# Kernel tuning notes

Hardware: AMD Instinct MI355X
Metric: run time of the kernel (lower is better)

Reference implementation:

```python
import jax, jax.numpy as jnp
import numpy as np

H = 128

def setup_inputs() -> dict:
    key = jax.random.key(0)
    kx, ke, ku, kub, kv, kvb = jax.random.split(key, 6)
    B, N = 8, 256
    s = 1.0 / np.sqrt(H)
    return {
        "x": jax.random.normal(kx, (B, N, H), dtype=jnp.float32),
        "e": jax.random.normal(ke, (B, N, N, H), dtype=jnp.float32),
        "U_w": jax.random.uniform(ku, (H, H), jnp.float32, -s, s),
        "U_b": jax.random.uniform(kub, (H,), jnp.float32, -s, s),
        "V_w": jax.random.uniform(kv, (H, H), jnp.float32, -s, s),
        "V_b": jax.random.uniform(kvb, (H,), jnp.float32, -s, s),
    }

def reference(x, e, U_w, U_b, V_w, V_b):
    # Ue: [B,N,N,H] = Linear(e); Vx: [B,N,H] = Linear(x)
    Ue = jnp.einsum('bijh,oh->bijo', e, U_w) + U_b
    Vx = jnp.einsum('bnh,oh->bno', x, V_w) + V_b
    # e_new[b,i,j] = Ue[b,i,j] + Vx[b,i] (rows) + Vx[b,j] (cols)
    e_new = Ue + Vx[:, :, None, :] + Vx[:, None, :, :]
    return e_new
```

## Files before the change

### kernel.cpp

```cpp
#include <hip/hip_runtime.h>
#include <hip/hip_bf16.h>


#define LDB 136

using bf16x8 = __attribute__((ext_vector_type(8))) short;
using f32x4  = __attribute__((ext_vector_type(4))) float;

__device__ inline bf16x8 pack8(const float4 a, const float4 b) {
  union { __hip_bfloat162 h2[4]; bf16x8 v; } u;
  u.h2[0] = __float22bfloat162_rn(make_float2(a.x, a.y));
  u.h2[1] = __float22bfloat162_rn(make_float2(a.z, a.w));
  u.h2[2] = __float22bfloat162_rn(make_float2(b.x, b.y));
  u.h2[3] = __float22bfloat162_rn(make_float2(b.z, b.w));
  return u.v;
}

__global__ __launch_bounds__(256) void vx_kernel(
    const float* __restrict__ x, const float* __restrict__ Vw,
    const float* __restrict__ Vb, const float* __restrict__ Ub,
    float* __restrict__ vx2) {
  __shared__ float xs[8][128];
  const int r0 = blockIdx.x * 8;
  for (int i = threadIdx.x; i < 8 * 32; i += 256)
    ((float4*)&xs[0][0])[i] = ((const float4*)(x + (size_t)r0 * 128))[i];
  __syncthreads();

  const int o    = threadIdx.x & 127;
  const int half = threadIdx.x >> 7;
  float acc[4] = {0.f, 0.f, 0.f, 0.f};
  const float4* vwrow = (const float4*)(Vw + (size_t)o * 128);
#pragma unroll 4
  for (int kc = 0; kc < 32; ++kc) {
    const float4 w4 = vwrow[kc];
#pragma unroll
    for (int r = 0; r < 4; ++r) {
      const float4 xv = ((const float4*)&xs[half * 4 + r][0])[kc];
      acc[r] += xv.x * w4.x + xv.y * w4.y + xv.z * w4.z + xv.w * w4.w;
    }
  }
  const float bias = Vb[o] + 0.5f * Ub[o];
#pragma unroll
  for (int r = 0; r < 4; ++r)
    vx2[(size_t)(r0 + half * 4 + r) * 128 + o] = acc[r] + bias;
}

__global__ __launch_bounds__(256) void edge_kernel(
    const float* __restrict__ e, const float* __restrict__ Uw,
    const float* __restrict__ vx2, float* __restrict__ out) {
  __shared__ alignas(16) __hip_bfloat16 As[64 * LDB];

  const int tid  = threadIdx.x;
  const int wave = tid >> 6;
  const int lane = tid & 63;
  const int ln   = lane & 15;
  const int kg   = lane >> 4;

  bf16x8 bfrag[2][4];
#pragma unroll
  for (int c = 0; c < 2; ++c) {
    const int o = 32 * wave + 16 * c + ln;
#pragma unroll
    for (int ks = 0; ks < 4; ++ks) {
      const float4* p = (const float4*)(Uw + (size_t)o * 128 + kg * 8 + ks * 32);
      bfrag[c][ks] = pack8(p[0], p[1]);
    }
  }

  const int nTiles = (8 * 256 * 256) / 64;
  for (int t = blockIdx.x; t < nTiles; t += gridDim.x) {
    const size_t rowBase = (size_t)t * 64;

    {
      const float4* src = (const float4*)(e + rowBase * 128);
      float4 f[8];
#pragma unroll
      for (int i = 0; i < 8; ++i) f[i] = src[i * 256 + tid];
#pragma unroll
      for (int i = 0; i < 8; ++i) {
        const int fi  = i * 256 + tid;
        const int row = fi >> 5;
        const int col = (fi & 31) * 4;
        union { __hip_bfloat162 h2[2]; unsigned long long u; } p;
        p.h2[0] = __float22bfloat162_rn(make_float2(f[i].x, f[i].y));
        p.h2[1] = __float22bfloat162_rn(make_float2(f[i].z, f[i].w));
        *(unsigned long long*)&As[row * LDB + col] = p.u;
      }
    }
    __syncthreads();

    f32x4 acc[4][2];
#pragma unroll
    for (int sub = 0; sub < 4; ++sub) {
      bf16x8 afrag[4];
#pragma unroll
      for (int ks = 0; ks < 4; ++ks)
        afrag[ks] = *(const bf16x8*)&As[(sub * 16 + ln) * LDB + kg * 8 + ks * 32];
#pragma unroll
      for (int c = 0; c < 2; ++c) {
        f32x4 a = {0.f, 0.f, 0.f, 0.f};
#pragma unroll
        for (int ks = 0; ks < 4; ++ks)
          a = __builtin_amdgcn_mfma_f32_16x16x32_bf16(afrag[ks], bfrag[c][ks], a, 0, 0, 0);
        acc[sub][c] = a;
      }
    }

#pragma unroll
    for (int sub = 0; sub < 4; ++sub) {
      const size_t rsub = rowBase + sub * 16;
      const int bi = (int)(rsub >> 8);
      const int b_ = (int)(rsub >> 16);
      const int j0 = (int)(rsub & 255);
      const int jr = b_ * 256 + j0;
#pragma unroll
      for (int c = 0; c < 2; ++c) {
        const int o = 32 * wave + 16 * c + ln;
        const float vxi = vx2[(size_t)bi * 128 + o];
#pragma unroll
        for (int reg = 0; reg < 4; ++reg) {
          const int rr = kg * 4 + reg;
          const float vxj = vx2[(size_t)(jr + rr) * 128 + o];
          out[(rsub + rr) * 128 + o] = acc[sub][c][reg] + vxi + vxj;
        }
      }
    }
    __syncthreads();
  }
}

extern "C" void kernel_launch(void* const* d_in, const int* in_sizes, int n_in,
                              void* d_out, int out_size, void* d_ws, size_t ws_size,
                              hipStream_t stream) {
  const float* x  = (const float*)d_in[0];
  const float* e  = (const float*)d_in[1];
  const float* Uw = (const float*)d_in[2];
  const float* Ub = (const float*)d_in[3];
  const float* Vw = (const float*)d_in[4];
  const float* Vb = (const float*)d_in[5];
  float* out = (float*)d_out;
  float* vx2 = (float*)d_ws;

  vx_kernel<<<256, 256, 0, stream>>>(x, Vw, Vb, Ub, vx2);
  edge_kernel<<<2048, 256, 0, stream>>>(e, Uw, vx2, out);
}
```

Before: 457.4 us.

## Give each wave an independent 16-row strip, loading A fragments straight into registers

The edge kernel no longer stages e tiles through LDS behind block-wide barriers. Each wave now owns 16-row strips, loads its A fragments directly from global memory into registers, and computes all 128 output columns. The U weights are held in LDS as pre-swizzled fragments, and the accumulators are seeded with the Vx row and column terms so no epilogue add is needed. This removes the per-tile __syncthreads and the LDS round-trip for the activations. The cost is more uncoalesced 32-byte global reads per lane and fewer rows in flight per block.

```diff
diff --git a/kernel.cpp b/kernel.cpp
--- a/kernel.cpp
+++ b/kernel.cpp
@@ -1,8 +1,6 @@
 #include <hip/hip_runtime.h>
 #include <hip/hip_bf16.h>
 
-
-#define LDB 136
 
 using bf16x8 = __attribute__((ext_vector_type(8))) short;
 using f32x4  = __attribute__((ext_vector_type(4))) float;
@@ -48,84 +46,79 @@
 __global__ __launch_bounds__(256) void edge_kernel(
     const float* __restrict__ e, const float* __restrict__ Uw,
     const float* __restrict__ vx2, float* __restrict__ out) {
-  __shared__ alignas(16) __hip_bfloat16 As[64 * LDB];
+  __shared__ alignas(16) bf16x8 Bs[8 * 4 * 64];
 
-  const int tid  = threadIdx.x;
+  const int tid = threadIdx.x;
+
+#pragma unroll
+  for (int k = 0; k < 8; ++k) {
+    const int idx  = tid + k * 256;
+    const int ll   = idx & 63;
+    const int ksi  = (idx >> 6) & 3;
+    const int cgi  = idx >> 8;
+    const int o    = cgi * 16 + (ll & 15);
+    const int kq   = ll >> 4;
+    const float4* p = (const float4*)(Uw + (size_t)o * 128 + ksi * 32 + kq * 8);
+    Bs[idx] = pack8(p[0], p[1]);
+  }
+  __syncthreads();
+
   const int wave = tid >> 6;
   const int lane = tid & 63;
   const int ln   = lane & 15;
   const int kg   = lane >> 4;
 
-  bf16x8 bfrag[2][4];
-#pragma unroll
-  for (int c = 0; c < 2; ++c) {
-    const int o = 32 * wave + 16 * c + ln;
+  const int gw = blockIdx.x * 4 + wave;
+  const int nw = gridDim.x * 4;
+  const int nStrips = (8 * 256 * 256) / 16;
+
+  for (int s = gw; s < nStrips; s += nw) {
+    const size_t rowBase = (size_t)s * 16;
+    const int bi = (int)(rowBase >> 8);
+    const int b_ = (int)(rowBase >> 16);
+    const int j0 = (int)(rowBase & 255);
+    const int jr = b_ * 256 + j0;
+
+    const float* arow = e + (rowBase + ln) * 128 + kg * 8;
+    float4 a0[4], a1[4];
 #pragma unroll
     for (int ks = 0; ks < 4; ++ks) {
-      const float4* p = (const float4*)(Uw + (size_t)o * 128 + kg * 8 + ks * 32);
-      bfrag[c][ks] = pack8(p[0], p[1]);
+      a0[ks] = *(const float4*)(arow + ks * 32);
+      a1[ks] = *(const float4*)(arow + ks * 32 + 4);
     }
-  }
 
-  const int nTiles = (8 * 256 * 256) / 64;
-  for (int t = blockIdx.x; t < nTiles; t += gridDim.x) {
-    const size_t rowBase = (size_t)t * 64;
+    f32x4 acc[8];
+#pragma unroll
+    for (int cg = 0; cg < 8; ++cg) {
+      const int o = cg * 16 + ln;
+      const float vxi = vx2[(size_t)bi * 128 + o];
+      const float* vj = vx2 + (size_t)(jr + kg * 4) * 128 + o;
+#pragma unroll
+      for (int reg = 0; reg < 4; ++reg)
+        acc[cg][reg] = vxi + vj[reg * 128];
+    }
 
-    {
-      const float4* src = (const float4*)(e + rowBase * 128);
-      float4 f[8];
+    bf16x8 af[4];
 #pragma unroll
-      for (int i = 0; i < 8; ++i) f[i] = src[i * 256 + tid];
+    for (int ks = 0; ks < 4; ++ks) af[ks] = pack8(a0[ks], a1[ks]);
+
 #pragma unroll
-      for (int i = 0; i < 8; ++i) {
-        const int fi  = i * 256 + tid;
-        const int row = fi >> 5;
-        const int col = (fi & 31) * 4;
-        union { __hip_bfloat162 h2[2]; unsigned long long u; } p;
-        p.h2[0] = __float22bfloat162_rn(make_float2(f[i].x, f[i].y));
-        p.h2[1] = __float22bfloat162_rn(make_float2(f[i].z, f[i].w));
-        *(unsigned long long*)&As[row * LDB + col] = p.u;
-      }
-    }
-    __syncthreads();
-
-    f32x4 acc[4][2];
-#pragma unroll
-    for (int sub = 0; sub < 4; ++sub) {
-      bf16x8 afrag[4];
+    for (int cg = 0; cg < 8; ++cg) {
+      const bf16x8* bp = &Bs[cg * 4 * 64 + lane];
+      f32x4 a = acc[cg];
 #pragma unroll
       for (int ks = 0; ks < 4; ++ks)
-        afrag[ks] = *(const bf16x8*)&As[(sub * 16 + ln) * LDB + kg * 8 + ks * 32];
-#pragma unroll
-      for (int c = 0; c < 2; ++c) {
-        f32x4 a = {0.f, 0.f, 0.f, 0.f};
-#pragma unroll
-        for (int ks = 0; ks < 4; ++ks)
-          a = __builtin_amdgcn_mfma_f32_16x16x32_bf16(afrag[ks], bfrag[c][ks], a, 0, 0, 0);
-        acc[sub][c] = a;
-      }
+        a = __builtin_amdgcn_mfma_f32_16x16x32_bf16(af[ks], bp[ks * 64], a, 0, 0, 0);
+      acc[cg] = a;
     }
 
+    float* orow = out + (rowBase + kg * 4) * 128 + ln;
 #pragma unroll
-    for (int sub = 0; sub < 4; ++sub) {
-      const size_t rsub = rowBase + sub * 16;
-      const int bi = (int)(rsub >> 8);
-      const int b_ = (int)(rsub >> 16);
-      const int j0 = (int)(rsub & 255);
-      const int jr = b_ * 256 + j0;
+    for (int cg = 0; cg < 8; ++cg) {
 #pragma unroll
-      for (int c = 0; c < 2; ++c) {
-        const int o = 32 * wave + 16 * c + ln;
-        const float vxi = vx2[(size_t)bi * 128 + o];
-#pragma unroll
-        for (int reg = 0; reg < 4; ++reg) {
-          const int rr = kg * 4 + reg;
-          const float vxj = vx2[(size_t)(jr + rr) * 128 + o];
-          out[(rsub + rr) * 128 + o] = acc[sub][c][reg] + vxi + vxj;
-        }
-      }
+      for (int reg = 0; reg < 4; ++reg)
+        orow[reg * 128 + cg * 16] = acc[cg][reg];
     }
-    __syncthreads();
   }
 }
 
```

Result: slower. 471.0 us (+3.0%).
